# Kernel tuning notes

Measured on AMD Instinct MI355X. Metric: run time of the kernel, lower is better.

## Reference

```python
import jax, jax.numpy as jnp
import numpy as np

B, N, M, H = 4, 1024, 1024, 64
IK, IQ, IV, IT = 3, 3, 5, 1


def _mlp(x, W1, b1, W2, b2):
    # Linear -> ReLU -> Linear  (matches torch.nn.Sequential in the module)
    return jax.nn.relu(x @ W1 + b1) @ W2 + b2


def setup_inputs() -> dict:
    key = jax.random.key(0)
    ks = jax.random.split(key, 18)
    rn = lambda k, s, sc: (jax.random.normal(k, s, jnp.float32) * sc)
    inp = {
        "coords_f": rn(ks[0], (B, N, IK), 1.0),
        "values_f": rn(ks[1], (B, N, IV), 1.0),
        "coords_t": rn(ks[2], (B, M, IQ), 1.0),
        # Wk MLP
        "Wk1": rn(ks[3], (IK, H), 1.0 / np.sqrt(IK)), "bk1": jnp.zeros((H,), jnp.float32),
        "Wk2": rn(ks[4], (H, H), 1.0 / np.sqrt(H)),   "bk2": jnp.zeros((H,), jnp.float32),
        # Wq MLP
        "Wq1": rn(ks[5], (IQ, H), 1.0 / np.sqrt(IQ)), "bq1": jnp.zeros((H,), jnp.float32),
        "Wq2": rn(ks[6], (H, H), 1.0 / np.sqrt(H)),   "bq2": jnp.zeros((H,), jnp.float32),
        # Wv MLP
        "Wv1": rn(ks[7], (IV, H), 1.0 / np.sqrt(IV)), "bv1": jnp.zeros((H,), jnp.float32),
        "Wv2": rn(ks[8], (H, H), 1.0 / np.sqrt(H)),   "bv2": jnp.zeros((H,), jnp.float32),
        # Output projection
        "Wo": rn(ks[9], (H, IT), 1.0 / np.sqrt(H)),   "bo": jnp.zeros((IT,), jnp.float32),
    }
    return inp


def reference(coords_f, values_f, coords_t,
              Wk1, bk1, Wk2, bk2,
              Wq1, bq1, Wq2, bq2,
              Wv1, bv1, Wv2, bv2,
              Wo, bo):
    K = _mlp(coords_f, Wk1, bk1, Wk2, bk2)   # [B, N, H]
    Q = _mlp(coords_t, Wq1, bq1, Wq2, bq2)   # [B, M, H]
    V = _mlp(values_f, Wv1, bv1, Wv2, bv2)   # [B, N, H]
    # L1 cdist: score[b, n, m] = sum_h |K[b,n,h] - Q[b,m,h]|
    score = jnp.abs(K[:, :, None, :] - Q[:, None, :, :]).sum(-1)  # [B, N, M]
    # custom NW kernel: softmax over keys (axis=1) of -d^2/2
    att = jax.nn.softmax(-0.5 * score * score, axis=1)            # [B, N, M]
    out = jnp.einsum('bnm,bnh->bmh', att, V)                      # [B, M, H]
    return out @ Wo + bo                                          # [B, M, IT]
```

## Files before the change

kernel.cpp:

```cpp
#include <hip/hip_runtime.h>
#include <math.h>

#define BB 4
#define NN 1024
#define MM 1024
#define HH 64
#define NT 8
#define BN 128
#define BM 64
#define MT (MM / BM)

static constexpr float NEG_BIG = -3.0e38f;
static constexpr float SCALE = -0.72134752044448170f;

__device__ __forceinline__ void gload16(const void* gsrc, void* lds_base) {
    __builtin_amdgcn_global_load_lds(
        (const __attribute__((address_space(1))) void*)gsrc,
        (__attribute__((address_space(3))) void*)lds_base,
        16, 0, 0);
}

__global__ __launch_bounds__(256)
void prep_kernel(const float* __restrict__ coords_f,
                 const float* __restrict__ values_f,
                 const float* __restrict__ coords_t,
                 const float* __restrict__ Wk1, const float* __restrict__ bk1,
                 const float* __restrict__ Wk2, const float* __restrict__ bk2,
                 const float* __restrict__ Wq1, const float* __restrict__ bq1,
                 const float* __restrict__ Wq2, const float* __restrict__ bq2,
                 const float* __restrict__ Wv1, const float* __restrict__ bv1,
                 const float* __restrict__ Wv2, const float* __restrict__ bv2,
                 const float* __restrict__ Wo,
                 float* __restrict__ Kout, float* __restrict__ Qout,
                 float* __restrict__ vhat) {
    const int bx = blockIdx.x;
    const int tid = threadIdx.x;

    if (bx < 512) {
        const int type = bx >> 8;
        const int sub = bx & 255;
        const int row = (sub >> 4) * 256 + tid;
        const int co  = (sub & 15) * 4;

        const float* in = type ? coords_t : coords_f;
        const float* W1 = type ? Wq1 : Wk1;
        const float* b1 = type ? bq1 : bk1;
        const float* W2 = type ? Wq2 : Wk2;
        const float* b2 = type ? bq2 : bk2;
        float* out = type ? Qout : Kout;

        const float in0 = in[row * 3 + 0];
        const float in1 = in[row * 3 + 1];
        const float in2 = in[row * 3 + 2];

        float acc[4];
#pragma unroll
        for (int j = 0; j < 4; ++j) acc[j] = b2[co + j];

#pragma unroll 4
        for (int hi = 0; hi < HH; ++hi) {
            float h = b1[hi];
            h = fmaf(in0, W1[hi], h);
            h = fmaf(in1, W1[64 + hi], h);
            h = fmaf(in2, W1[128 + hi], h);
            h = fmaxf(h, 0.0f);
            const float* w = W2 + hi * 64 + co;
#pragma unroll
            for (int j = 0; j < 4; ++j) acc[j] = fmaf(h, w[j], acc[j]);
        }
        float4* o = reinterpret_cast<float4*>(out + row * 64 + co);
        *o = make_float4(acc[0], acc[1], acc[2], acc[3]);
    } else {
        const int sub = bx - 512;
        __shared__ float w2o[64];
        __shared__ float b2o_sh;
        if (tid < 64) {
            float s = 0.0f;
            for (int ho = 0; ho < 64; ++ho) s = fmaf(Wv2[tid * 64 + ho], Wo[ho], s);
            w2o[tid] = s;
        }
        if (tid == 0) {
            float s = 0.0f;
            for (int ho = 0; ho < 64; ++ho) s = fmaf(bv2[ho], Wo[ho], s);
            b2o_sh = s;
        }
        __syncthreads();

        const int row = sub * 256 + tid;
        const float* vin = values_f + row * 5;
        const float i0 = vin[0], i1 = vin[1], i2 = vin[2], i3 = vin[3], i4 = vin[4];

        float s = b2o_sh;
        for (int j = 0; j < HH; ++j) {
            float h = bv1[j];
            h = fmaf(i0, Wv1[j], h);
            h = fmaf(i1, Wv1[64 + j], h);
            h = fmaf(i2, Wv1[128 + j], h);
            h = fmaf(i3, Wv1[192 + j], h);
            h = fmaf(i4, Wv1[256 + j], h);
            h = fmaxf(h, 0.0f);
            s = fmaf(h, w2o[j], s);
        }
        vhat[row] = s;
    }
}

__global__ __launch_bounds__(256, 2)
void fused_kernel(const float* __restrict__ Kb,
                  const float* __restrict__ Qb,
                  const float* __restrict__ vh,
                  float* __restrict__ mxp,
                  float* __restrict__ denp,
                  float* __restrict__ nump) {
    __shared__ float kt[BN * 64];
    __shared__ float qt[BM * 64];
    __shared__ float red[16 * 64 * 3];

    const int tid = threadIdx.x;
    const int nt = blockIdx.x, mt = blockIdx.y, b = blockIdx.z;
    const int n0 = nt * BN, m0 = mt * BM;
    const int ty = tid >> 4, tx = tid & 15;
    const int wv = tid >> 6;

    const float4* ksrc = reinterpret_cast<const float4*>(Kb + (b * NN + n0) * 64);
    const float4* qsrc = reinterpret_cast<const float4*>(Qb + (b * MM + m0) * 64);

#pragma unroll
    for (int l = 0; l < 8; ++l) {
        const int fidx = l * 256 + tid;
        const int row = fidx >> 4, col = fidx & 15;
        gload16(ksrc + row * 16 + (col ^ (row & 7)), kt + (l * 256 + wv * 64) * 4);
    }
#pragma unroll
    for (int l = 0; l < 4; ++l) {
        const int fidx = l * 256 + tid;
        const int row = fidx >> 4, col = fidx & 15;
        gload16(qsrc + row * 16 + (col ^ (row & 7)), qt + (l * 256 + wv * 64) * 4);
    }

    float vloc[8];
#pragma unroll
    for (int ni = 0; ni < 8; ++ni) vloc[ni] = vh[b * NN + n0 + ni * 16 + ty];

    __syncthreads();

    const float4* kt4 = reinterpret_cast<const float4*>(kt);
    const float4* qt4 = reinterpret_cast<const float4*>(qt);
    const int swk = ty & 7;
    const int swq = tx & 7;
    const float4* kbase = kt4 + ty * 16;
    const float4* qbase = qt4 + tx * 16;

    float acc[8][4];
#pragma unroll
    for (int i = 0; i < 8; ++i)
#pragma unroll
        for (int j = 0; j < 4; ++j) acc[i][j] = 0.0f;

#pragma unroll
    for (int h4 = 0; h4 < 16; ++h4) {
        float4 kv[8], qv[4];
        const int ck = h4 ^ swk;
        const int cq = h4 ^ swq;
#pragma unroll
        for (int ni = 0; ni < 8; ++ni)
            kv[ni] = kbase[ni * 256 + ck];
#pragma unroll
        for (int mj = 0; mj < 4; ++mj)
            qv[mj] = qbase[mj * 256 + cq];
#pragma unroll
        for (int ni = 0; ni < 8; ++ni)
#pragma unroll
            for (int mj = 0; mj < 4; ++mj) {
                acc[ni][mj] += fabsf(kv[ni].x - qv[mj].x);
                acc[ni][mj] += fabsf(kv[ni].y - qv[mj].y);
                acc[ni][mj] += fabsf(kv[ni].z - qv[mj].z);
                acc[ni][mj] += fabsf(kv[ni].w - qv[mj].w);
            }
    }

    float mxr[4], denr[4], numr[4];
#pragma unroll
    for (int mj = 0; mj < 4; ++mj) {
        float a[8];
#pragma unroll
        for (int ni = 0; ni < 8; ++ni) {
            const float d = acc[ni][mj];
            a[ni] = d * d * SCALE;
        }
        const float mx = fmaxf(fmaxf(fmaxf(a[0], a[1]), fmaxf(a[2], a[3])),
                               fmaxf(fmaxf(a[4], a[5]), fmaxf(a[6], a[7])));
        float den = 0.0f, num = 0.0f;
#pragma unroll
        for (int ni = 0; ni < 8; ++ni) {
            const float p = __builtin_amdgcn_exp2f(a[ni] - mx);
            den += p;
            num = fmaf(p, vloc[ni], num);
        }
        mxr[mj] = mx; denr[mj] = den; numr[mj] = num;
    }

#pragma unroll
    for (int mj = 0; mj < 4; ++mj) {
        const int base = (ty * 64 + mj * 16 + tx) * 3;
        red[base + 0] = mxr[mj];
        red[base + 1] = denr[mj];
        red[base + 2] = numr[mj];
    }
    __syncthreads();

    if (tid < 64) {
        float M = NEG_BIG, D = 0.0f, Nu = 0.0f;
        for (int t = 0; t < 16; ++t) {
            const int base = (t * 64 + tid) * 3;
            const float m2 = red[base + 0];
            const float d2 = red[base + 1];
            const float n2 = red[base + 2];
            const float nm = fmaxf(M, m2);
            const float s0 = __builtin_amdgcn_exp2f(M - nm);
            const float s1 = __builtin_amdgcn_exp2f(m2 - nm);
            D  = D * s0 + d2 * s1;
            Nu = Nu * s0 + n2 * s1;
            M = nm;
        }
        const int p = nt * (BB * MM) + b * MM + m0 + tid;
        mxp[p] = M; denp[p] = D; nump[p] = Nu;
    }
}

__global__ __launch_bounds__(64)
void combine_kernel(const float* __restrict__ mxp,
                    const float* __restrict__ denp,
                    const float* __restrict__ nump,
                    const float* __restrict__ bo,
                    float* __restrict__ out) {
    const int bm = blockIdx.x * 64 + threadIdx.x;
    float m[NT], d[NT], n[NT];
#pragma unroll
    for (int t = 0; t < NT; ++t) {
        const int idx = t * (BB * MM) + bm;
        m[t] = mxp[idx];
        d[t] = denp[idx];
        n[t] = nump[idx];
    }
    const float M = fmaxf(fmaxf(fmaxf(m[0], m[1]), fmaxf(m[2], m[3])),
                          fmaxf(fmaxf(m[4], m[5]), fmaxf(m[6], m[7])));
    float D = 0.0f, Nu = 0.0f;
#pragma unroll
    for (int t = 0; t < NT; ++t) {
        const float s = __builtin_amdgcn_exp2f(m[t] - M);
        D  = fmaf(d[t], s, D);
        Nu = fmaf(n[t], s, Nu);
    }
    out[bm] = Nu / D + bo[0];
}

extern "C" void kernel_launch(void* const* d_in, const int* in_sizes, int n_in,
                              void* d_out, int out_size, void* d_ws, size_t ws_size,
                              hipStream_t stream) {
    const float* coords_f = (const float*)d_in[0];
    const float* values_f = (const float*)d_in[1];
    const float* coords_t = (const float*)d_in[2];
    const float* Wk1 = (const float*)d_in[3];
    const float* bk1 = (const float*)d_in[4];
    const float* Wk2 = (const float*)d_in[5];
    const float* bk2 = (const float*)d_in[6];
    const float* Wq1 = (const float*)d_in[7];
    const float* bq1 = (const float*)d_in[8];
    const float* Wq2 = (const float*)d_in[9];
    const float* bq2 = (const float*)d_in[10];
    const float* Wv1 = (const float*)d_in[11];
    const float* bv1 = (const float*)d_in[12];
    const float* Wv2 = (const float*)d_in[13];
    const float* bv2 = (const float*)d_in[14];
    const float* Wo  = (const float*)d_in[15];
    const float* bo  = (const float*)d_in[16];

    float* ws  = (float*)d_ws;
    float* Kb  = ws;
    float* Qb  = Kb + BB * NN * HH;
    float* vh  = Qb + BB * MM * HH;
    float* mxp = vh + BB * NN;
    float* denp = mxp + NT * BB * MM;
    float* nump = denp + NT * BB * MM;

    prep_kernel<<<dim3(528), 256, 0, stream>>>(
        coords_f, values_f, coords_t,
        Wk1, bk1, Wk2, bk2, Wq1, bq1, Wq2, bq2,
        Wv1, bv1, Wv2, bv2, Wo, Kb, Qb, vh);

    fused_kernel<<<dim3(NT, MT, BB), 256, 0, stream>>>(
        Kb, Qb, vh, mxp, denp, nump);

    combine_kernel<<<dim3(64), 64, 0, stream>>>(
        mxp, denp, nump, bo, (float*)d_out);
}
```

Before: 27.81 us.

## Stage MLP weights in LDS and double-buffer LDS loads in distance loop

The prep kernel now stages W1/b1 rows and the per-block W2 column slice into shared memory as float4s, so each thread stops re-reading scattered global weights. The main L1-distance loop is also restructured to double-buffer its K/Q register loads from LDS, issuing the next slice's loads before computing the current one, so LDS latency overlaps with ALU work. The cost is higher register pressure from two sets of K/Q buffers, which could lower occupancy.

```diff
diff --git a/kernel.cpp b/kernel.cpp
--- a/kernel.cpp
+++ b/kernel.cpp
@@ -49,27 +49,34 @@
         const float* b2 = type ? bq2 : bk2;
         float* out = type ? Qout : Kout;
 
+        __shared__ float4 hrow[64];
+        __shared__ float4 w2c[64];
+        if (tid < 64) {
+            hrow[tid] = make_float4(W1[tid], W1[64 + tid], W1[128 + tid], b1[tid]);
+        } else if (tid < 128) {
+            const int hi = tid - 64;
+            w2c[hi] = *reinterpret_cast<const float4*>(W2 + hi * 64 + co);
+        }
+        __syncthreads();
+
         const float in0 = in[row * 3 + 0];
         const float in1 = in[row * 3 + 1];
         const float in2 = in[row * 3 + 2];
 
-        float acc[4];
-#pragma unroll
-        for (int j = 0; j < 4; ++j) acc[j] = b2[co + j];
-
-#pragma unroll 4
+        float acc0 = b2[co + 0], acc1 = b2[co + 1], acc2 = b2[co + 2], acc3 = b2[co + 3];
+
+#pragma unroll 8
         for (int hi = 0; hi < HH; ++hi) {
-            float h = b1[hi];
-            h = fmaf(in0, W1[hi], h);
-            h = fmaf(in1, W1[64 + hi], h);
-            h = fmaf(in2, W1[128 + hi], h);
+            const float4 hr = hrow[hi];
+            const float4 w  = w2c[hi];
+            float h = fmaf(in0, hr.x, fmaf(in1, hr.y, fmaf(in2, hr.z, hr.w)));
             h = fmaxf(h, 0.0f);
-            const float* w = W2 + hi * 64 + co;
-#pragma unroll
-            for (int j = 0; j < 4; ++j) acc[j] = fmaf(h, w[j], acc[j]);
-        }
-        float4* o = reinterpret_cast<float4*>(out + row * 64 + co);
-        *o = make_float4(acc[0], acc[1], acc[2], acc[3]);
+            acc0 = fmaf(h, w.x, acc0);
+            acc1 = fmaf(h, w.y, acc1);
+            acc2 = fmaf(h, w.z, acc2);
+            acc3 = fmaf(h, w.w, acc3);
+        }
+        *reinterpret_cast<float4*>(out + row * 64 + co) = make_float4(acc0, acc1, acc2, acc3);
     } else {
         const int sub = bx - 512;
         __shared__ float w2o[64];
@@ -157,17 +164,17 @@
 #pragma unroll
         for (int j = 0; j < 4; ++j) acc[i][j] = 0.0f;
 
-#pragma unroll
-    for (int h4 = 0; h4 < 16; ++h4) {
-        float4 kv[8], qv[4];
+    auto loadK = [&](float4 (&kv)[8], int h4) {
         const int ck = h4 ^ swk;
+#pragma unroll
+        for (int ni = 0; ni < 8; ++ni) kv[ni] = kbase[ni * 256 + ck];
+    };
+    auto loadQ = [&](float4 (&qv)[4], int h4) {
         const int cq = h4 ^ swq;
 #pragma unroll
-        for (int ni = 0; ni < 8; ++ni)
-            kv[ni] = kbase[ni * 256 + ck];
-#pragma unroll
-        for (int mj = 0; mj < 4; ++mj)
-            qv[mj] = qbase[mj * 256 + cq];
+        for (int mj = 0; mj < 4; ++mj) qv[mj] = qbase[mj * 256 + cq];
+    };
+    auto compute = [&](const float4 (&kv)[8], const float4 (&qv)[4]) {
 #pragma unroll
         for (int ni = 0; ni < 8; ++ni)
 #pragma unroll
@@ -177,6 +184,16 @@
                 acc[ni][mj] += fabsf(kv[ni].z - qv[mj].z);
                 acc[ni][mj] += fabsf(kv[ni].w - qv[mj].w);
             }
+    };
+
+    float4 kvA[8], qvA[4], kvB[8], qvB[4];
+    loadK(kvA, 0); loadQ(qvA, 0);
+#pragma unroll
+    for (int h4 = 0; h4 < 16; h4 += 2) {
+        loadK(kvB, h4 + 1); loadQ(qvB, h4 + 1);
+        compute(kvA, qvA);
+        if (h4 + 2 < 16) { loadK(kvA, h4 + 2); loadQ(qvA, h4 + 2); }
+        compute(kvB, qvB);
     }
 
     float mxr[4], denr[4], numr[4];
```

Result: no change. 27.50 us (-1.1%).
